# Kernel optimization log

Hardware: AMD Instinct MI355X
Metric: run time of the kernel (lower is better)

The kernel has to match this reference:

```python
import jax, jax.numpy as jnp
import numpy as np

N_NODES = 50000
NEG_SLOPE = 0.2  # PyG GATConv default LeakyReLU slope


def gat_conv(x, src, dst, W, att_src, att_dst, bias, heads, out_ch, concat):
    """PyG-style GATConv (dropout=0, add_self_loops omitted to match raw edge list usage).
    x: [N, in], W: [in, heads*out_ch], att_*: [1, heads, out_ch], bias: [heads*out_ch] or [out_ch].
    Messages flow src -> dst; softmax normalizes over incoming edges of each dst node."""
    N = x.shape[0]
    h = (x @ W).reshape(N, heads, out_ch)                      # [N,H,C]
    a_s = (h * att_src).sum(-1)                                # [N,H]
    a_d = (h * att_dst).sum(-1)                                # [N,H]
    e = jax.nn.leaky_relu(a_s[src] + a_d[dst], NEG_SLOPE)      # [E,H] per-edge logits
    m = jax.ops.segment_max(e, dst, num_segments=N)            # [N,H] stable softmax max
    p = jnp.exp(e - m[dst])                                    # [E,H]
    s = jax.ops.segment_sum(p, dst, num_segments=N)            # [N,H]
    alpha = p / (s[dst] + 1e-16)                               # [E,H] attention coeffs
    out = jax.ops.segment_sum(h[src] * alpha[:, :, None], dst, num_segments=N)  # [N,H,C]
    out = out.reshape(N, heads * out_ch) if concat else out.mean(axis=1)
    return out + bias


def setup_inputs() -> dict:
    key = jax.random.key(0)
    ks = jax.random.split(key, 10)
    in_ch, hid, heads, out_ch = 128, 32, 4, 64
    E = 800000
    x = jax.random.normal(ks[0], (N_NODES, in_ch), dtype=jnp.float32)
    edge_index = jax.random.randint(ks[1], (2, E), 0, N_NODES, dtype=jnp.int64)
    sc = 0.1
    return {
        "x": x,
        "edge_index": edge_index,
        "W1": jax.random.normal(ks[2], (in_ch, heads * hid), dtype=jnp.float32) * sc,
        "att_src1": jax.random.normal(ks[3], (1, heads, hid), dtype=jnp.float32) * sc,
        "att_dst1": jax.random.normal(ks[4], (1, heads, hid), dtype=jnp.float32) * sc,
        "b1": jnp.zeros((heads * hid,), dtype=jnp.float32),
        "W2": jax.random.normal(ks[5], (heads * hid, out_ch), dtype=jnp.float32) * sc,
        "att_src2": jax.random.normal(ks[6], (1, 1, out_ch), dtype=jnp.float32) * sc,
        "att_dst2": jax.random.normal(ks[7], (1, 1, out_ch), dtype=jnp.float32) * sc,
        "b2": jnp.zeros((out_ch,), dtype=jnp.float32),
    }


def reference(x, edge_index, W1, att_src1, att_dst1, b1, W2, att_src2, att_dst2, b2):
    src, dst = edge_index[0], edge_index[1]
    h = gat_conv(x, src, dst, W1, att_src1, att_dst1, b1, heads=4, out_ch=32, concat=True)
    h = jax.nn.elu(h)
    out = gat_conv(h, src, dst, W2, att_src2, att_dst2, b2, heads=1, out_ch=64, concat=False)
    return out
```

## Files before the change

### kernel.cpp

```cpp
#include <hip/hip_runtime.h>

#define N_NODES 50000
#define N_EDGES 800000
#define GEMM_BLKS ((N_NODES + 63) / 64)
#define NGRP 8
#define RANGE ((N_NODES + NGRP - 1) / NGRP)
#define FILL_BLKS 4096
#define EDGES_PER_BLK 1564
#define MAXDEG 64
#define AGG_BLKS (N_NODES / 2)

typedef __attribute__((ext_vector_type(8))) short bf16x8;
typedef __attribute__((ext_vector_type(4))) float f32x4;
typedef unsigned short u16;
typedef unsigned int u32;

__device__ __forceinline__ float lrelu(float x) { return x > 0.f ? x : 0.2f * x; }

__device__ __forceinline__ u16 f2bf(float f) {
    u32 u = __float_as_uint(f);
    return (u16)((u + 0x7FFFu + ((u >> 16) & 1u)) >> 16);
}
__device__ __forceinline__ float bflo(u32 w) { return __uint_as_float(w << 16); }
__device__ __forceinline__ float bfhi(u32 w) { return __uint_as_float(w & 0xFFFF0000u); }
__device__ __forceinline__ float elu(float x) { return x > 0.f ? x : __expf(x) - 1.f; }

__global__ __launch_bounds__(256) void k_fill(
    const int* __restrict__ src, const int* __restrict__ dst,
    int* __restrict__ deg, int* __restrict__ col)
{
    const int g = blockIdx.x & 7;
    const int b = blockIdx.x >> 3;
    const int lo = g * RANGE;
    const int hi = min(lo + RANGE, N_NODES);
    const int e0 = b * EDGES_PER_BLK;
    const int e1 = min(e0 + EDGES_PER_BLK, N_EDGES);
    for (int e = e0 + threadIdx.x; e < e1; e += 256) {
        int v = dst[e];
        if (v >= lo && v < hi) {
            int pos = atomicAdd(&deg[v], 1);
            if (pos < MAXDEG) col[v * MAXDEG + pos] = src[e];
        }
    }
}

__global__ __launch_bounds__(256) void k_prep(
    const float* __restrict__ W1, const float* __restrict__ as1v, const float* __restrict__ ad1v,
    const float* __restrict__ W2, const float* __restrict__ as2v, const float* __restrict__ ad2v,
    u16* __restrict__ Wt1, u16* __restrict__ Wt2)
{
    int gid = blockIdx.x * 256 + threadIdx.x;
    if (gid < 144 * 128) {
        int n = gid >> 7, k = gid & 127;
        float v = 0.f;
        if (n < 128) v = W1[k * 128 + n];
        else if (n < 136) {
            int h = n - 128;
            const float* att = (h < 4) ? as1v : ad1v;
            int hh = h & 3;
            float s = 0.f;
            for (int c = 0; c < 32; ++c) s += W1[k * 128 + hh * 32 + c] * att[hh * 32 + c];
            v = s;
        }
        Wt1[n * 128 + k] = f2bf(v);
    } else {
        int g2 = gid - 144 * 128;
        if (g2 < 80 * 128) {
            int n = g2 >> 7, k = g2 & 127;
            float v = 0.f;
            if (n < 64) v = W2[k * 64 + n];
            else if (n == 64) { float s = 0.f; for (int c = 0; c < 64; ++c) s += W2[k * 64 + c] * as2v[c]; v = s; }
            else if (n == 65) { float s = 0.f; for (int c = 0; c < 64; ++c) s += W2[k * 64 + c] * ad2v[c]; v = s; }
            Wt2[n * 128 + k] = f2bf(v);
        }
    }
}

__global__ __launch_bounds__(256) void k_gemm1(
    const float* __restrict__ x, const u16* __restrict__ Wt1,
    u16* __restrict__ hbf, float* __restrict__ as_, float* __restrict__ ad_)
{
    __shared__ u16 xs[64][136];
    __shared__ u16 ws[144][136];
    const int t = threadIdx.x;
    const int n0 = blockIdx.x * 64;
    #pragma unroll
    for (int it = 0; it < 8; ++it) {
        int idx = it * 256 + t;
        int row = idx >> 5, c4 = (idx & 31) * 4;
        int n = n0 + row;
        float4 xv = make_float4(0.f, 0.f, 0.f, 0.f);
        if (n < N_NODES) xv = *(const float4*)&x[(size_t)n * 128 + c4];
        uint2 pk;
        pk.x = (u32)f2bf(xv.x) | ((u32)f2bf(xv.y) << 16);
        pk.y = (u32)f2bf(xv.z) | ((u32)f2bf(xv.w) << 16);
        *(uint2*)&xs[row][c4] = pk;
    }
    #pragma unroll
    for (int it = 0; it < 9; ++it) {
        int idx = it * 256 + t;
        int row = idx >> 4, c8 = (idx & 15) * 8;
        *(uint4*)&ws[row][c8] = *(const uint4*)&Wt1[row * 128 + c8];
    }
    __syncthreads();
    const int l = t & 63, w = t >> 6;
    const int lm = l & 15, quad = l >> 4;
    f32x4 acc[9];
    #pragma unroll
    for (int nt = 0; nt < 9; ++nt) acc[nt] = (f32x4){0.f, 0.f, 0.f, 0.f};
    const u16* arow = &xs[w * 16 + lm][0];
    #pragma unroll
    for (int kc = 0; kc < 4; ++kc) {
        int k0 = kc * 32 + quad * 8;
        bf16x8 a = *(const bf16x8*)&arow[k0];
        #pragma unroll
        for (int nt = 0; nt < 9; ++nt) {
            bf16x8 b = *(const bf16x8*)&ws[nt * 16 + lm][k0];
            acc[nt] = __builtin_amdgcn_mfma_f32_16x16x32_bf16(a, b, acc[nt], 0, 0, 0);
        }
    }
    #pragma unroll
    for (int r = 0; r < 4; ++r) {
        int n = n0 + w * 16 + quad * 4 + r;
        if (n >= N_NODES) continue;
        #pragma unroll
        for (int nt = 0; nt < 8; ++nt)
            hbf[(size_t)n * 128 + nt * 16 + lm] = f2bf(acc[nt][r]);
        if (lm < 4)      as_[n * 4 + lm]     = acc[8][r];
        else if (lm < 8) ad_[n * 4 + lm - 4] = acc[8][r];
    }
}

__global__ __launch_bounds__(256) void k_agg1(
    const int* __restrict__ deg, const int* __restrict__ col,
    const float* __restrict__ as_, const float* __restrict__ ad_,
    const u32* __restrict__ h1u, const float* __restrict__ b1,
    u32* __restrict__ out1u)
{
    __shared__ int scol[2][MAXDEG];
    __shared__ float4 sp[2][MAXDEG];
    __shared__ float racc[2][9][16];
    const int t = threadIdx.x;
    const int unit = t >> 7;
    const int tu = t & 127;
    const int v = blockIdx.x * 2 + unit;
    const int w = tu >> 6;
    const int l = tu & 63;
    const int slot = l >> 4;
    const int c = l & 15;
    const int hh = c >> 2;
    const int gs = w * 4 + slot;
    const int dg = min(deg[v], MAXDEG);
    const float4 adv = ((const float4*)ad_)[v];
    if (tu < dg) {
        int u = col[v * MAXDEG + tu];
        scol[unit][tu] = u;
        float4 aa = ((const float4*)as_)[u];
        float4 p;
        p.x = __expf(lrelu(aa.x + adv.x));
        p.y = __expf(lrelu(aa.y + adv.y));
        p.z = __expf(lrelu(aa.z + adv.z));
        p.w = __expf(lrelu(aa.w + adv.w));
        sp[unit][tu] = p;
    }
    __syncthreads();
    float a[8] = {0.f, 0.f, 0.f, 0.f, 0.f, 0.f, 0.f, 0.f};
    float s = 0.f;
    for (int i0 = gs; i0 < dg; i0 += 16) {
        int i1 = i0 + 8;
        bool m1 = i1 < dg;
        int u0 = scol[unit][i0];
        int u1 = scol[unit][m1 ? i1 : i0];
        float p0 = ((const float*)&sp[unit][i0])[hh];
        float p1 = m1 ? ((const float*)&sp[unit][i1])[hh] : 0.f;
        uint4 w0 = *(const uint4*)(h1u + (u0 << 6) + (c << 2));
        uint4 w1 = *(const uint4*)(h1u + (u1 << 6) + (c << 2));
        a[0] = fmaf(p0, bflo(w0.x), a[0]); a[1] = fmaf(p0, bfhi(w0.x), a[1]);
        a[2] = fmaf(p0, bflo(w0.y), a[2]); a[3] = fmaf(p0, bfhi(w0.y), a[3]);
        a[4] = fmaf(p0, bflo(w0.z), a[4]); a[5] = fmaf(p0, bfhi(w0.z), a[5]);
        a[6] = fmaf(p0, bflo(w0.w), a[6]); a[7] = fmaf(p0, bfhi(w0.w), a[7]);
        a[0] = fmaf(p1, bflo(w1.x), a[0]); a[1] = fmaf(p1, bfhi(w1.x), a[1]);
        a[2] = fmaf(p1, bflo(w1.y), a[2]); a[3] = fmaf(p1, bfhi(w1.y), a[3]);
        a[4] = fmaf(p1, bflo(w1.z), a[4]); a[5] = fmaf(p1, bfhi(w1.z), a[5]);
        a[6] = fmaf(p1, bflo(w1.w), a[6]); a[7] = fmaf(p1, bfhi(w1.w), a[7]);
        s += p0 + p1;
    }
    #pragma unroll
    for (int k = 0; k < 8; ++k) {
        a[k] += __shfl_xor(a[k], 16);
        a[k] += __shfl_xor(a[k], 32);
    }
    s += __shfl_xor(s, 16);
    s += __shfl_xor(s, 32);
    if (w == 1 && slot == 0) {
        #pragma unroll
        for (int k = 0; k < 8; ++k) racc[unit][k][c] = a[k];
        racc[unit][8][c] = s;
    }
    __syncthreads();
    if (w == 0 && slot == 0) {
        #pragma unroll
        for (int k = 0; k < 8; ++k) a[k] += racc[unit][k][c];
        s += racc[unit][8][c];
        float inv = 1.f / (s + 1e-16f);
        float4 b0 = *(const float4*)&b1[8 * c];
        float4 b4 = *(const float4*)&b1[8 * c + 4];
        float o0 = elu(a[0] * inv + b0.x);
        float o1 = elu(a[1] * inv + b0.y);
        float o2 = elu(a[2] * inv + b0.z);
        float o3 = elu(a[3] * inv + b0.w);
        float o4 = elu(a[4] * inv + b4.x);
        float o5 = elu(a[5] * inv + b4.y);
        float o6 = elu(a[6] * inv + b4.z);
        float o7 = elu(a[7] * inv + b4.w);
        uint4 pk;
        pk.x = (u32)f2bf(o0) | ((u32)f2bf(o1) << 16);
        pk.y = (u32)f2bf(o2) | ((u32)f2bf(o3) << 16);
        pk.z = (u32)f2bf(o4) | ((u32)f2bf(o5) << 16);
        pk.w = (u32)f2bf(o6) | ((u32)f2bf(o7) << 16);
        *(uint4*)(out1u + v * 64 + 4 * c) = pk;
    }
}

__global__ __launch_bounds__(256) void k_gemm2(
    const u16* __restrict__ xbf, const u16* __restrict__ Wt2,
    u16* __restrict__ hbf, float* __restrict__ as_, float* __restrict__ ad_)
{
    __shared__ u16 xs[64][136];
    __shared__ u16 ws[80][136];
    const int t = threadIdx.x;
    const int n0 = blockIdx.x * 64;
    #pragma unroll
    for (int it = 0; it < 4; ++it) {
        int idx = it * 256 + t;
        int row = idx >> 4, c8 = (idx & 15) * 8;
        int n = n0 + row;
        uint4 vv = make_uint4(0u, 0u, 0u, 0u);
        if (n < N_NODES) vv = *(const uint4*)&xbf[(size_t)n * 128 + c8];
        *(uint4*)&xs[row][c8] = vv;
    }
    #pragma unroll
    for (int it = 0; it < 5; ++it) {
        int idx = it * 256 + t;
        int row = idx >> 4, c8 = (idx & 15) * 8;
        *(uint4*)&ws[row][c8] = *(const uint4*)&Wt2[row * 128 + c8];
    }
    __syncthreads();
    const int l = t & 63, w = t >> 6;
    const int lm = l & 15, quad = l >> 4;
    f32x4 acc[5];
    #pragma unroll
    for (int nt = 0; nt < 5; ++nt) acc[nt] = (f32x4){0.f, 0.f, 0.f, 0.f};
    const u16* arow = &xs[w * 16 + lm][0];
    #pragma unroll
    for (int kc = 0; kc < 4; ++kc) {
        int k0 = kc * 32 + quad * 8;
        bf16x8 a = *(const bf16x8*)&arow[k0];
        #pragma unroll
        for (int nt = 0; nt < 5; ++nt) {
            bf16x8 b = *(const bf16x8*)&ws[nt * 16 + lm][k0];
            acc[nt] = __builtin_amdgcn_mfma_f32_16x16x32_bf16(a, b, acc[nt], 0, 0, 0);
        }
    }
    #pragma unroll
    for (int r = 0; r < 4; ++r) {
        int n = n0 + w * 16 + quad * 4 + r;
        if (n >= N_NODES) continue;
        #pragma unroll
        for (int nt = 0; nt < 4; ++nt)
            hbf[(size_t)n * 64 + nt * 16 + lm] = f2bf(acc[nt][r]);
        if (lm == 0)      as_[n] = acc[4][r];
        else if (lm == 1) ad_[n] = acc[4][r];
    }
}

__global__ __launch_bounds__(128) void k_agg2(
    const int* __restrict__ deg, const int* __restrict__ col,
    const float* __restrict__ as_, const float* __restrict__ ad_,
    const u32* __restrict__ h2u, const float* __restrict__ b2,
    float* __restrict__ out)
{
    __shared__ int scol[2][MAXDEG];
    __shared__ float sp[2][MAXDEG];
    const int t = threadIdx.x;
    const int unit = t >> 6;
    const int l = t & 63;
    const int v = blockIdx.x * 2 + unit;
    const int slot = l >> 3;
    const int c = l & 7;
    const int dg = min(deg[v], MAXDEG);
    const float adv = ad_[v];
    if (l < dg) {
        int u = col[v * MAXDEG + l];
        scol[unit][l] = u;
        sp[unit][l] = __expf(lrelu(as_[u] + adv));
    }
    __syncthreads();
    float a[8] = {0.f, 0.f, 0.f, 0.f, 0.f, 0.f, 0.f, 0.f};
    float s = 0.f;
    for (int i0 = slot; i0 < dg; i0 += 16) {
        int i1 = i0 + 8;
        bool m1 = i1 < dg;
        int u0 = scol[unit][i0];
        int u1 = scol[unit][m1 ? i1 : i0];
        float p0 = sp[unit][i0];
        float p1 = m1 ? sp[unit][i1] : 0.f;
        uint4 w0 = *(const uint4*)(h2u + (u0 << 5) + (c << 2));
        uint4 w1 = *(const uint4*)(h2u + (u1 << 5) + (c << 2));
        a[0] = fmaf(p0, bflo(w0.x), a[0]); a[1] = fmaf(p0, bfhi(w0.x), a[1]);
        a[2] = fmaf(p0, bflo(w0.y), a[2]); a[3] = fmaf(p0, bfhi(w0.y), a[3]);
        a[4] = fmaf(p0, bflo(w0.z), a[4]); a[5] = fmaf(p0, bfhi(w0.z), a[5]);
        a[6] = fmaf(p0, bflo(w0.w), a[6]); a[7] = fmaf(p0, bfhi(w0.w), a[7]);
        a[0] = fmaf(p1, bflo(w1.x), a[0]); a[1] = fmaf(p1, bfhi(w1.x), a[1]);
        a[2] = fmaf(p1, bflo(w1.y), a[2]); a[3] = fmaf(p1, bfhi(w1.y), a[3]);
        a[4] = fmaf(p1, bflo(w1.z), a[4]); a[5] = fmaf(p1, bfhi(w1.z), a[5]);
        a[6] = fmaf(p1, bflo(w1.w), a[6]); a[7] = fmaf(p1, bfhi(w1.w), a[7]);
        s += p0 + p1;
    }
    #pragma unroll
    for (int k = 0; k < 8; ++k) {
        a[k] += __shfl_xor(a[k], 8);
        a[k] += __shfl_xor(a[k], 16);
        a[k] += __shfl_xor(a[k], 32);
    }
    s += __shfl_xor(s, 8);
    s += __shfl_xor(s, 16);
    s += __shfl_xor(s, 32);
    if (slot == 0) {
        float inv = 1.f / (s + 1e-16f);
        float4 b0 = *(const float4*)&b2[8 * c];
        float4 b4 = *(const float4*)&b2[8 * c + 4];
        float4 oa, ob;
        oa.x = a[0] * inv + b0.x;
        oa.y = a[1] * inv + b0.y;
        oa.z = a[2] * inv + b0.z;
        oa.w = a[3] * inv + b0.w;
        ob.x = a[4] * inv + b4.x;
        ob.y = a[5] * inv + b4.y;
        ob.z = a[6] * inv + b4.z;
        ob.w = a[7] * inv + b4.w;
        *(float4*)&out[(size_t)v * 64 + 8 * c]     = oa;
        *(float4*)&out[(size_t)v * 64 + 8 * c + 4] = ob;
    }
}

extern "C" void kernel_launch(void* const* d_in, const int* in_sizes, int n_in,
                              void* d_out, int out_size, void* d_ws, size_t ws_size,
                              hipStream_t stream)
{
    const float* x      = (const float*)d_in[0];
    const int*   ei     = (const int*)d_in[1];
    const float* W1     = (const float*)d_in[2];
    const float* att_s1 = (const float*)d_in[3];
    const float* att_d1 = (const float*)d_in[4];
    const float* b1     = (const float*)d_in[5];
    const float* W2     = (const float*)d_in[6];
    const float* att_s2 = (const float*)d_in[7];
    const float* att_d2 = (const float*)d_in[8];
    const float* b2     = (const float*)d_in[9];
    const int* src = ei;
    const int* dst = ei + N_EDGES;
    float* out = (float*)d_out;

    char* wsp = (char*)d_ws;
    u16* Wt1   = (u16*)wsp;  wsp += 144 * 128 * 2;
    u16* Wt2   = (u16*)wsp;  wsp += 80 * 128 * 2;
    u16* h1bf  = (u16*)wsp;  wsp += (size_t)N_NODES * 128 * 2;
    u16* o1bf  = (u16*)wsp;  wsp += (size_t)N_NODES * 128 * 2;
    u16* h2bf  = (u16*)wsp;  wsp += (size_t)N_NODES * 64 * 2;
    float* as1 = (float*)wsp; wsp += (size_t)N_NODES * 4 * 4;
    float* ad1 = (float*)wsp; wsp += (size_t)N_NODES * 4 * 4;
    float* as2 = (float*)wsp; wsp += (size_t)N_NODES * 4;
    float* ad2 = (float*)wsp; wsp += (size_t)N_NODES * 4;
    int* deg   = (int*)wsp;   wsp += (size_t)N_NODES * 4;
    int* col   = (int*)wsp;   wsp += (size_t)N_NODES * MAXDEG * 4;

    k_prep<<<112, 256, 0, stream>>>(W1, att_s1, att_d1, W2, att_s2, att_d2, Wt1, Wt2);
    hipMemsetAsync(deg, 0, (size_t)N_NODES * 4, stream);
    k_fill<<<FILL_BLKS, 256, 0, stream>>>(src, dst, deg, col);

    k_gemm1<<<GEMM_BLKS, 256, 0, stream>>>(x, Wt1, h1bf, as1, ad1);
    k_agg1<<<AGG_BLKS, 256, 0, stream>>>(deg, col, as1, ad1, (const u32*)h1bf, b1, (u32*)o1bf);

    k_gemm2<<<GEMM_BLKS, 256, 0, stream>>>(o1bf, Wt2, h2bf, as2, ad2);
    k_agg2<<<AGG_BLKS, 128, 0, stream>>>(deg, col, as2, ad2, (const u32*)h2bf, b2, out);
}
```

Measured before the change: 215.4 us.

## Use one wavefront per node in aggregation kernels, dropping shared memory and barriers

Both aggregation kernels now give each destination node a single 64-lane wavefront instead of two waves (agg1) or a shared-memory staging pass. Lanes read column indices and compute the exp attention weights inline, so the shared-memory staging, the cross-wave reduction and the __syncthreads are gone. The cost is redundant loads of col/as_ and redundant exp work across the lanes that share an edge, plus fewer lanes in flight per node in agg1.

```diff
diff --git a/kernel.cpp b/kernel.cpp
--- a/kernel.cpp
+++ b/kernel.cpp
@@ -8,7 +8,7 @@
 #define FILL_BLKS 4096
 #define EDGES_PER_BLK 1564
 #define MAXDEG 64
-#define AGG_BLKS (N_NODES / 2)
+#define AGG_BLKS (N_NODES / 4)
 
 typedef __attribute__((ext_vector_type(8))) short bf16x8;
 typedef __attribute__((ext_vector_type(4))) float f32x4;
@@ -137,42 +137,25 @@
     const u32* __restrict__ h1u, const float* __restrict__ b1,
     u32* __restrict__ out1u)
 {
-    __shared__ int scol[2][MAXDEG];
-    __shared__ float4 sp[2][MAXDEG];
-    __shared__ float racc[2][9][16];
     const int t = threadIdx.x;
-    const int unit = t >> 7;
-    const int tu = t & 127;
-    const int v = blockIdx.x * 2 + unit;
-    const int w = tu >> 6;
-    const int l = tu & 63;
+    const int wv = t >> 6;
+    const int l = t & 63;
+    const int v = blockIdx.x * 4 + wv;
+    const int c = l & 15;
     const int slot = l >> 4;
-    const int c = l & 15;
     const int hh = c >> 2;
-    const int gs = w * 4 + slot;
     const int dg = min(deg[v], MAXDEG);
-    const float4 adv = ((const float4*)ad_)[v];
-    if (tu < dg) {
-        int u = col[v * MAXDEG + tu];
-        scol[unit][tu] = u;
-        float4 aa = ((const float4*)as_)[u];
-        float4 p;
-        p.x = __expf(lrelu(aa.x + adv.x));
-        p.y = __expf(lrelu(aa.y + adv.y));
-        p.z = __expf(lrelu(aa.z + adv.z));
-        p.w = __expf(lrelu(aa.w + adv.w));
-        sp[unit][tu] = p;
-    }
-    __syncthreads();
+    const float adh = ad_[v * 4 + hh];
+    const int base = v * MAXDEG;
     float a[8] = {0.f, 0.f, 0.f, 0.f, 0.f, 0.f, 0.f, 0.f};
     float s = 0.f;
-    for (int i0 = gs; i0 < dg; i0 += 16) {
-        int i1 = i0 + 8;
+    for (int i0 = slot; i0 < dg; i0 += 8) {
+        int i1 = i0 + 4;
         bool m1 = i1 < dg;
-        int u0 = scol[unit][i0];
-        int u1 = scol[unit][m1 ? i1 : i0];
-        float p0 = ((const float*)&sp[unit][i0])[hh];
-        float p1 = m1 ? ((const float*)&sp[unit][i1])[hh] : 0.f;
+        int u0 = col[base + i0];
+        int u1 = col[base + (m1 ? i1 : i0)];
+        float p0 = __expf(lrelu(as_[u0 * 4 + hh] + adh));
+        float p1 = m1 ? __expf(lrelu(as_[u1 * 4 + hh] + adh)) : 0.f;
         uint4 w0 = *(const uint4*)(h1u + (u0 << 6) + (c << 2));
         uint4 w1 = *(const uint4*)(h1u + (u1 << 6) + (c << 2));
         a[0] = fmaf(p0, bflo(w0.x), a[0]); a[1] = fmaf(p0, bfhi(w0.x), a[1]);
@@ -192,16 +175,7 @@
     }
     s += __shfl_xor(s, 16);
     s += __shfl_xor(s, 32);
-    if (w == 1 && slot == 0) {
-        #pragma unroll
-        for (int k = 0; k < 8; ++k) racc[unit][k][c] = a[k];
-        racc[unit][8][c] = s;
-    }
-    __syncthreads();
-    if (w == 0 && slot == 0) {
-        #pragma unroll
-        for (int k = 0; k < 8; ++k) a[k] += racc[unit][k][c];
-        s += racc[unit][8][c];
+    if (slot == 0) {
         float inv = 1.f / (s + 1e-16f);
         float4 b0 = *(const float4*)&b1[8 * c];
         float4 b4 = *(const float4*)&b1[8 * c + 4];
@@ -274,37 +248,30 @@
     }
 }
 
-__global__ __launch_bounds__(128) void k_agg2(
+__global__ __launch_bounds__(256) void k_agg2(
     const int* __restrict__ deg, const int* __restrict__ col,
     const float* __restrict__ as_, const float* __restrict__ ad_,
     const u32* __restrict__ h2u, const float* __restrict__ b2,
     float* __restrict__ out)
 {
-    __shared__ int scol[2][MAXDEG];
-    __shared__ float sp[2][MAXDEG];
     const int t = threadIdx.x;
-    const int unit = t >> 6;
+    const int wv = t >> 6;
     const int l = t & 63;
-    const int v = blockIdx.x * 2 + unit;
+    const int v = blockIdx.x * 4 + wv;
+    const int c = l & 7;
     const int slot = l >> 3;
-    const int c = l & 7;
     const int dg = min(deg[v], MAXDEG);
-    const float adv = ad_[v];
-    if (l < dg) {
-        int u = col[v * MAXDEG + l];
-        scol[unit][l] = u;
-        sp[unit][l] = __expf(lrelu(as_[u] + adv));
-    }
-    __syncthreads();
+    const float adh = ad_[v];
+    const int base = v * MAXDEG;
     float a[8] = {0.f, 0.f, 0.f, 0.f, 0.f, 0.f, 0.f, 0.f};
     float s = 0.f;
     for (int i0 = slot; i0 < dg; i0 += 16) {
         int i1 = i0 + 8;
         bool m1 = i1 < dg;
-        int u0 = scol[unit][i0];
-        int u1 = scol[unit][m1 ? i1 : i0];
-        float p0 = sp[unit][i0];
-        float p1 = m1 ? sp[unit][i1] : 0.f;
+        int u0 = col[base + i0];
+        int u1 = col[base + (m1 ? i1 : i0)];
+        float p0 = __expf(lrelu(as_[u0] + adh));
+        float p1 = m1 ? __expf(lrelu(as_[u1] + adh)) : 0.f;
         uint4 w0 = *(const uint4*)(h2u + (u0 << 5) + (c << 2));
         uint4 w1 = *(const uint4*)(h2u + (u1 << 5) + (c << 2));
         a[0] = fmaf(p0, bflo(w0.x), a[0]); a[1] = fmaf(p0, bfhi(w0.x), a[1]);
@@ -383,5 +350,5 @@
     k_agg1<<<AGG_BLKS, 256, 0, stream>>>(deg, col, as1, ad1, (const u32*)h1bf, b1, (u32*)o1bf);
 
     k_gemm2<<<GEMM_BLKS, 256, 0, stream>>>(o1bf, Wt2, h2bf, as2, ad2);
-    k_agg2<<<AGG_BLKS, 128, 0, stream>>>(deg, col, as2, ad2, (const u32*)h2bf, b2, out);
-}
+    k_agg2<<<AGG_BLKS, 256, 0, stream>>>(deg, col, as2, ad2, (const u32*)h2bf, b2, out);
+}
```

Result: faster. 208.7 us (-3.1%).
